# Kernel optimization log

Measured on AMD Instinct MI355X. Metric: run time of the kernel, lower is better.

## Reference

```python
import jax, jax.numpy as jnp
import numpy as np

B, D_MODEL, N, H = 2, 1024, 2048, 16
HEAD_DIM = D_MODEL // H  # 64


def _proj(x, W, b):
    # Conv1d kernel_size=1 == per-position GEMM over channels. x: [B, Cin, N]
    return jnp.einsum('oi,bin->bon', W, x) + b[:, None]


def setup_inputs() -> dict:
    key = jax.random.key(0)
    ks = jax.random.split(key, 11)
    s = 1.0 / np.sqrt(D_MODEL)
    mk = lambda k: (jax.random.uniform(k, (D_MODEL, D_MODEL), jnp.float32, -s, s))
    return {
        'query': jax.random.normal(ks[0], (B, D_MODEL, N), jnp.float32),
        'key': jax.random.normal(ks[1], (B, D_MODEL, N), jnp.float32),
        'value': jax.random.normal(ks[2], (B, D_MODEL, N), jnp.float32),
        'Wq': mk(ks[3]), 'bq': jax.random.uniform(ks[4], (D_MODEL,), jnp.float32, -s, s),
        'Wk': mk(ks[5]), 'bk': jax.random.uniform(ks[6], (D_MODEL,), jnp.float32, -s, s),
        'Wv': mk(ks[7]), 'bv': jax.random.uniform(ks[8], (D_MODEL,), jnp.float32, -s, s),
        'Wm': mk(ks[9]), 'bm': jax.random.uniform(ks[10], (D_MODEL,), jnp.float32, -s, s),
    }


def reference(query, key, value, Wq, bq, Wk, bk, Wv, bv, Wm, bm):
    b = query.shape[0]
    # project then split channels as (head_dim, heads) exactly like torch .view
    q = _proj(query, Wq, bq).reshape(b, HEAD_DIM, H, -1)  # [B, d, H, N]
    k = _proj(key, Wk, bk).reshape(b, HEAD_DIM, H, -1)
    v = _proj(value, Wv, bv).reshape(b, HEAD_DIM, H, -1)
    scores = jnp.einsum('bdhn,bdhm->bhnm', q, k) / np.sqrt(HEAD_DIM).astype(np.float32)
    prob = jax.nn.softmax(scores, axis=-1)  # [B, H, N, N]
    x = jnp.einsum('bhnm,bdhm->bdhn', prob, v)  # [B, d, H, N]
    return _proj(x.reshape(b, D_MODEL, -1), Wm, bm)  # [B, d_model, N]
```

## Files before the change

kernel.cpp:

```cpp
#include <hip/hip_runtime.h>
#include <hip/hip_bf16.h>
#include <stdint.h>

#define DM 1024
#define NS 2048
#define NH 16
#define HD 64

typedef unsigned short u16;
typedef __attribute__((ext_vector_type(8))) short short8;
typedef __attribute__((ext_vector_type(4))) short s16x4;
typedef __attribute__((ext_vector_type(8))) unsigned short u16x8;
typedef __attribute__((ext_vector_type(4))) float f32x4;
typedef __attribute__((ext_vector_type(4))) unsigned short u16x4;

#define MFMA_PV(a, b, c) __builtin_amdgcn_mfma_f32_16x16x16bf16_1k(a, b, c, 0, 0, 0)

static __device__ __forceinline__ u16 f2bf(float f) {
  union { float f; uint32_t i; } x; x.f = f;
  return (u16)((x.i + 0x7fffu + ((x.i >> 16) & 1u)) >> 16);
}
static __device__ __forceinline__ uint32_t pkbf(float a, float b) {
  union { __hip_bfloat162 h; uint32_t u; } cv;
  cv.h = __float22bfloat162_rn(float2{a, b});
  return cv.u;
}
static __device__ __forceinline__ u16x4 pkbf4(float a, float b, float c, float d) {
  union { uint32_t u[2]; u16x4 v; } cv;
  cv.u[0] = pkbf(a, b); cv.u[1] = pkbf(c, d);
  return cv.v;
}
static __device__ __forceinline__ s16x4 pkbf4s(float a, float b, float c, float d) {
  union { uint32_t u[2]; s16x4 v; } cv;
  cv.u[0] = pkbf(a, b); cv.u[1] = pkbf(c, d);
  return cv.v;
}
static __device__ __forceinline__ void gload16(u16* lds, const u16* g) {
  auto l = (__attribute__((address_space(3))) uint32_t*)(uint32_t)(uintptr_t)lds;
  auto gp = (const __attribute__((address_space(1))) uint32_t*)(uintptr_t)g;
  __builtin_amdgcn_global_load_lds(gp, l, 16, 0, 0);
}

__global__ __launch_bounds__(256) void cvt4_k(const float* __restrict__ a,
                                              const float* __restrict__ b,
                                              const float* __restrict__ c,
                                              const float* __restrict__ d,
                                              u16* __restrict__ oa, u16* __restrict__ ob,
                                              u16* __restrict__ oc, u16* __restrict__ od) {
  const int y = blockIdx.y;
  const float* in = y == 0 ? a : y == 1 ? b : y == 2 ? c : d;
  u16* out = y == 0 ? oa : y == 1 ? ob : y == 2 ? oc : od;
  int i = (blockIdx.x * 256 + threadIdx.x) * 4;
  f32x4 v = *(const f32x4*)(in + i);
  *(u16x4*)(out + i) = pkbf4(v.x, v.y, v.z, v.w);
}

__global__ __launch_bounds__(256) void trf3_k(const float* __restrict__ q,
                                              const float* __restrict__ k,
                                              const float* __restrict__ v,
                                              u16* __restrict__ oq, u16* __restrict__ ok,
                                              u16* __restrict__ ov) {
  __shared__ __attribute__((aligned(16))) u16 t[64][65];
  const int z = blockIdx.z, b = z & 1, which = z >> 1;
  const float* in = which == 0 ? q : which == 1 ? k : v;
  u16* out = which == 0 ? oq : which == 1 ? ok : ov;
  const float* ip = in + (size_t)b * DM * NS;
  u16* op = out + (size_t)b * DM * NS;
  const int r0 = blockIdx.y * 64, c0 = blockIdx.x * 64;
  const int tx = threadIdx.x, ty = threadIdx.y;
#pragma unroll
  for (int j = 0; j < 4; ++j) {
    int row = ty + j * 16;
    f32x4 vv = *(const f32x4*)(ip + (size_t)(r0 + row) * NS + c0 + tx * 4);
    u16x4 bb = pkbf4(vv.x, vv.y, vv.z, vv.w);
    t[row][tx * 4 + 0] = bb.x; t[row][tx * 4 + 1] = bb.y;
    t[row][tx * 4 + 2] = bb.z; t[row][tx * 4 + 3] = bb.w;
  }
  __syncthreads();
#pragma unroll
  for (int j = 0; j < 4; ++j) {
    int crow = ty + j * 16;
    u16x4 vv;
    vv.x = t[tx * 4 + 0][crow]; vv.y = t[tx * 4 + 1][crow];
    vv.z = t[tx * 4 + 2][crow]; vv.w = t[tx * 4 + 3][crow];
    *(u16x4*)(op + (size_t)(c0 + crow) * DM + r0 + tx * 4) = vv;
  }
}

__global__ __launch_bounds__(256) void tr_k(const u16* __restrict__ in,
                                            u16* __restrict__ out) {
  __shared__ __attribute__((aligned(16))) u16 t[64][65];
  const int b = blockIdx.z;
  const u16* ip = in + (size_t)b * DM * NS;
  u16* op = out + (size_t)b * DM * NS;
  const int r0 = blockIdx.y * 64, c0 = blockIdx.x * 64;
  const int tx = threadIdx.x, ty = threadIdx.y;
#pragma unroll
  for (int j = 0; j < 4; ++j) {
    int row = ty + j * 16;
    u16x4 v = *(const u16x4*)(ip + (size_t)(r0 + row) * NS + c0 + tx * 4);
    t[row][tx * 4 + 0] = v.x; t[row][tx * 4 + 1] = v.y;
    t[row][tx * 4 + 2] = v.z; t[row][tx * 4 + 3] = v.w;
  }
  __syncthreads();
#pragma unroll
  for (int j = 0; j < 4; ++j) {
    int crow = ty + j * 16;
    u16x4 v;
    v.x = t[tx * 4 + 0][crow]; v.y = t[tx * 4 + 1][crow];
    v.z = t[tx * 4 + 2][crow]; v.w = t[tx * 4 + 3][crow];
    *(u16x4*)(op + (size_t)(c0 + crow) * DM + r0 + tx * 4) = v;
  }
}

__global__ __launch_bounds__(256) void qkv_k(
    const u16* __restrict__ Xq, const u16* __restrict__ Xk, const u16* __restrict__ Xv,
    const u16* __restrict__ Wq, const u16* __restrict__ Wk, const u16* __restrict__ Wv,
    const float* __restrict__ bq, const float* __restrict__ bk, const float* __restrict__ bv,
    u16* __restrict__ QH, u16* __restrict__ KH, u16* __restrict__ VH) {
  __shared__ __attribute__((aligned(16))) u16 As[128 * 32];
  __shared__ __attribute__((aligned(16))) u16 Bs[128 * 32];
  const int z = blockIdx.z, b = z & 1, which = z >> 1;
  const u16* X = which == 0 ? Xq : which == 1 ? Xk : Xv;
  const u16* W = which == 0 ? Wq : which == 1 ? Wk : Wv;
  const float* bias = which == 0 ? bq : which == 1 ? bk : bv;
  u16* out = which == 0 ? QH : which == 1 ? KH : VH;
  const float sc = which == 0 ? 0.18033688011112042f : 1.0f;
  const int m0 = blockIdx.x * 128;
  const int c0 = blockIdx.y * 128;
  const u16* Xb = X + (size_t)b * NS * DM;
  const int tid = threadIdx.x;
  const int lane = tid & 63, w = tid >> 6;
  const int wm = w >> 1, wc = w & 1;
  const int qd = lane >> 4, ml = lane & 15;
  const int sml = (ml >> 1) & 3;

  f32x4 acc[4][4];
#pragma unroll
  for (int i = 0; i < 4; ++i)
#pragma unroll
    for (int j = 0; j < 4; ++j) acc[i][j] = (f32x4){0.f, 0.f, 0.f, 0.f};

  for (int k0 = 0; k0 < DM; k0 += 32) {
    __syncthreads();
#pragma unroll
    for (int it = 0; it < 2; ++it) {
      int ci = it * 256 + tid;
      int row = ci >> 2;
      int jg = (ci & 3) ^ ((ci >> 3) & 3);
      gload16(&As[ci * 8], Xb + (size_t)(m0 + row) * DM + k0 + jg * 8);
      gload16(&Bs[ci * 8], W + (size_t)(c0 + row) * DM + k0 + jg * 8);
    }
    __syncthreads();
    short8 af[4], bf[4];
#pragma unroll
    for (int i = 0; i < 4; ++i) {
      af[i] = *(const short8*)&As[(wm * 64 + i * 16 + ml) * 32 + ((qd ^ sml) * 8)];
      bf[i] = *(const short8*)&Bs[(wc * 64 + i * 16 + ml) * 32 + ((qd ^ sml) * 8)];
    }
#pragma unroll
    for (int mi = 0; mi < 4; ++mi)
#pragma unroll
      for (int ci2 = 0; ci2 < 4; ++ci2)
        acc[mi][ci2] = __builtin_amdgcn_mfma_f32_16x16x32_bf16(af[mi], bf[ci2],
                                                               acc[mi][ci2], 0, 0, 0);
  }

  const int cw = c0 + wc * 64;
  const int mw = m0 + wm * 64;
  float bv4[4];
#pragma unroll
  for (int ci2 = 0; ci2 < 4; ++ci2) bv4[ci2] = bias[cw + ci2 * 16 + ml];

  if (which < 2) {
    const int h = ml, d0 = cw >> 4;
    u16* ob = out + ((size_t)(b * NH + h) * NS) * HD;
#pragma unroll
    for (int mi = 0; mi < 4; ++mi) {
#pragma unroll
      for (int r = 0; r < 4; ++r) {
        int n = mw + mi * 16 + qd * 4 + r;
        *(u16x4*)(ob + (size_t)n * HD + d0) =
            pkbf4((acc[mi][0][r] + bv4[0]) * sc, (acc[mi][1][r] + bv4[1]) * sc,
                  (acc[mi][2][r] + bv4[2]) * sc, (acc[mi][3][r] + bv4[3]) * sc);
      }
    }
  } else {
#pragma unroll
    for (int ci2 = 0; ci2 < 4; ++ci2) {
      int c = cw + ci2 * 16 + ml;
      int h = c & 15, d = c >> 4;
#pragma unroll
      for (int mi = 0; mi < 4; ++mi) {
        int nb = mw + mi * 16 + qd * 4;
        *(u16x4*)(out + ((size_t)(b * NH + h) * HD + d) * NS + nb) =
            pkbf4(acc[mi][ci2][0] + bv4[ci2], acc[mi][ci2][1] + bv4[ci2],
                  acc[mi][ci2][2] + bv4[ci2], acc[mi][ci2][3] + bv4[ci2]);
      }
    }
  }
}

__global__ __launch_bounds__(256) void proj_o(const u16* __restrict__ X,
                                              const u16* __restrict__ W,
                                              const float* __restrict__ bias,
                                              float* __restrict__ out) {
  __shared__ __attribute__((aligned(16))) u16 As[64 * 32];
  __shared__ __attribute__((aligned(16))) u16 Bs[128 * 32];
  const int b = blockIdx.z;
  const int m0 = blockIdx.x * 64;
  const int c0 = blockIdx.y * 128;
  const u16* Xb = X + (size_t)b * NS * DM;
  const int tid = threadIdx.x;
  const int lane = tid & 63, w = tid >> 6;
  const int wm = w >> 1, wc = w & 1;
  const int qd = lane >> 4, ml = lane & 15;
  const int sml = (ml >> 1) & 3;

  f32x4 acc[2][4];
#pragma unroll
  for (int i = 0; i < 2; ++i)
#pragma unroll
    for (int j = 0; j < 4; ++j) acc[i][j] = (f32x4){0.f, 0.f, 0.f, 0.f};

  for (int k0 = 0; k0 < DM; k0 += 32) {
    __syncthreads();
    {
      int jg = (tid & 3) ^ ((tid >> 3) & 3);
      int row = tid >> 2;
      gload16(&As[tid * 8], Xb + (size_t)(m0 + row) * DM + k0 + jg * 8);
    }
#pragma unroll
    for (int it = 0; it < 2; ++it) {
      int ci = it * 256 + tid;
      int row = ci >> 2;
      int jg = (ci & 3) ^ ((ci >> 3) & 3);
      gload16(&Bs[ci * 8], W + (size_t)(c0 + row) * DM + k0 + jg * 8);
    }
    __syncthreads();
    short8 af[2], bf[4];
#pragma unroll
    for (int i = 0; i < 2; ++i)
      af[i] = *(const short8*)&As[(wm * 32 + i * 16 + ml) * 32 + ((qd ^ sml) * 8)];
#pragma unroll
    for (int i = 0; i < 4; ++i)
      bf[i] = *(const short8*)&Bs[(wc * 64 + i * 16 + ml) * 32 + ((qd ^ sml) * 8)];
#pragma unroll
    for (int mi = 0; mi < 2; ++mi)
#pragma unroll
      for (int ci2 = 0; ci2 < 4; ++ci2)
        acc[mi][ci2] = __builtin_amdgcn_mfma_f32_16x16x32_bf16(af[mi], bf[ci2],
                                                               acc[mi][ci2], 0, 0, 0);
  }

  const int cw = c0 + wc * 64;
  const int mw = m0 + wm * 32;
#pragma unroll
  for (int ci2 = 0; ci2 < 4; ++ci2) {
    int c = cw + ci2 * 16 + ml;
    float bv = bias[c];
#pragma unroll
    for (int mi = 0; mi < 2; ++mi) {
      int nb = mw + mi * 16 + qd * 4;
      f32x4 v;
      v.x = acc[mi][ci2][0] + bv; v.y = acc[mi][ci2][1] + bv;
      v.z = acc[mi][ci2][2] + bv; v.w = acc[mi][ci2][3] + bv;
      *(f32x4*)(out + ((size_t)b * DM + c) * NS + nb) = v;
    }
  }
}

__global__ __launch_bounds__(256) void attn_k(const u16* __restrict__ Q,
                                              const u16* __restrict__ K,
                                              const u16* __restrict__ V,
                                              u16* __restrict__ XO) {
  __shared__ __attribute__((aligned(16))) u16 Ks[2 * 2 * 2048];
  __shared__ __attribute__((aligned(16))) u16 Vs[2 * 2 * 2048];
  const int bh = blockIdx.y, b = bh >> 4, h = bh & 15;
  const int n0 = blockIdx.x * 64;
  const u16* Qb = Q + (size_t)bh * NS * HD;
  const u16* Kb = K + (size_t)bh * NS * HD;
  const u16* Vb = V + (size_t)bh * HD * NS;
  const int tid = threadIdx.x, lane = tid & 63, w = tid >> 6;
  const int qd = lane >> 4, ml = lane & 15;
  const int sml = (ml >> 1) & 3;

  short8 aq[2];
  {
    const u16* qr = Qb + (size_t)(n0 + w * 16 + ml) * HD + qd * 8;
    aq[0] = *(const short8*)qr;
    aq[1] = *(const short8*)(qr + 32);
  }

  const int srow = tid >> 2;
  const int jg = (tid & 3) ^ ((tid >> 3) & 3);

#pragma unroll
  for (int s = 0; s < 2; ++s) {
    gload16(&Ks[s * 2048 + tid * 8], Kb + (size_t)srow * HD + s * 32 + jg * 8);
    gload16(&Vs[s * 2048 + tid * 8], Vb + (size_t)srow * NS + s * 32 + jg * 8);
  }
  __syncthreads();

  f32x4 O[4];
#pragma unroll
  for (int i = 0; i < 4; ++i) O[i] = (f32x4){0.f, 0.f, 0.f, 0.f};
  f32x4 lsum4 = (f32x4){0.f, 0.f, 0.f, 0.f};

  for (int kb = 0; kb < NS / 64; ++kb) {
    const int cur = kb & 1, nxt = cur ^ 1;
    if (kb < NS / 64 - 1) {
#pragma unroll
      for (int s = 0; s < 2; ++s) {
        gload16(&Ks[(nxt * 2 + s) * 2048 + tid * 8],
                Kb + (size_t)((kb + 1) * 64 + srow) * HD + s * 32 + jg * 8);
        gload16(&Vs[(nxt * 2 + s) * 2048 + tid * 8],
                Vb + (size_t)srow * NS + (kb + 1) * 64 + s * 32 + jg * 8);
      }
    }

    const u16* kbase = &Ks[cur * 2 * 2048];
    f32x4 S[4];
#pragma unroll
    for (int f = 0; f < 4; ++f) S[f] = (f32x4){0.f, 0.f, 0.f, 0.f};
#pragma unroll
    for (int f = 0; f < 4; ++f)
#pragma unroll
      for (int ks = 0; ks < 2; ++ks) {
        short8 bk = *(const short8*)&kbase[ks * 2048 + (f * 16 + ml) * 32 +
                                           ((qd ^ sml) * 8)];
        S[f] = __builtin_amdgcn_mfma_f32_16x16x32_bf16(bk, aq[ks], S[f], 0, 0, 0);
      }

    s16x4 pf[4];
#pragma unroll
    for (int f = 0; f < 4; ++f) {
      f32x4 p;
      p.x = __builtin_amdgcn_exp2f(S[f][0]);
      p.y = __builtin_amdgcn_exp2f(S[f][1]);
      p.z = __builtin_amdgcn_exp2f(S[f][2]);
      p.w = __builtin_amdgcn_exp2f(S[f][3]);
      lsum4 += p;
      pf[f] = pkbf4s(p.x, p.y, p.z, p.w);
    }

    const u16* vbase = &Vs[cur * 2 * 2048];
#pragma unroll
    for (int t = 0; t < 4; ++t) {
      const int vs = t >> 1;
      const int voff = ((((t & 1) * 2 + (qd >> 1)) ^ sml) * 8) + (qd & 1) * 4;
#pragma unroll
      for (int df = 0; df < 4; ++df) {
        s16x4 vb = *(const s16x4*)&vbase[vs * 2048 + (df * 16 + ml) * 32 + voff];
        O[df] = MFMA_PV(pf[t], vb, O[df]);
      }
    }
    __syncthreads();
  }

  float lsum = (lsum4.x + lsum4.y) + (lsum4.z + lsum4.w);
  lsum += __shfl_xor(lsum, 16);
  lsum += __shfl_xor(lsum, 32);
  float linv[4];
#pragma unroll
  for (int r = 0; r < 4; ++r) linv[r] = 1.f / __shfl(lsum, qd * 4 + r);

  const int nb = n0 + w * 16 + qd * 4;
#pragma unroll
  for (int df = 0; df < 4; ++df) {
    int d = df * 16 + ml;
    int c = d * NH + h;
    *(u16x4*)(XO + ((size_t)b * DM + c) * NS + nb) =
        pkbf4(O[df][0] * linv[0], O[df][1] * linv[1],
              O[df][2] * linv[2], O[df][3] * linv[3]);
  }
}

extern "C" void kernel_launch(void* const* d_in, const int* in_sizes, int n_in,
                              void* d_out, int out_size, void* d_ws, size_t ws_size,
                              hipStream_t stream) {
  const float* query = (const float*)d_in[0];
  const float* key = (const float*)d_in[1];
  const float* value = (const float*)d_in[2];
  const float* Wq = (const float*)d_in[3]; const float* bq = (const float*)d_in[4];
  const float* Wk = (const float*)d_in[5]; const float* bk = (const float*)d_in[6];
  const float* Wv = (const float*)d_in[7]; const float* bv = (const float*)d_in[8];
  const float* Wm = (const float*)d_in[9]; const float* bm = (const float*)d_in[10];

  u16* ws = (u16*)d_ws;
  const size_t TS = (size_t)2 * NS * DM;
  const size_t WSZ = (size_t)DM * DM;
  u16* XTq = ws;
  u16* XTk = ws + TS;
  u16* XTv = ws + 2 * TS;
  u16* QH = ws + 3 * TS;
  u16* KH = ws + 4 * TS;
  u16* VH = ws + 5 * TS;
  u16* Wqb = ws + 6 * TS;
  u16* Wkb = Wqb + WSZ;
  u16* Wvb = Wkb + WSZ;
  u16* Wmb = Wvb + WSZ;
  u16* XO = XTq;
  u16* XOT = XTk;

  cvt4_k<<<dim3(WSZ / 1024, 4), 256, 0, stream>>>(Wq, Wk, Wv, Wm, Wqb, Wkb, Wvb, Wmb);

  dim3 tb(16, 16);
  trf3_k<<<dim3(NS / 64, DM / 64, 6), tb, 0, stream>>>(query, key, value, XTq, XTk, XTv);

  qkv_k<<<dim3(NS / 128, DM / 128, 6), 256, 0, stream>>>(
      XTq, XTk, XTv, Wqb, Wkb, Wvb, bq, bk, bv, QH, KH, VH);

  attn_k<<<dim3(NS / 64, 32), 256, 0, stream>>>(QH, KH, VH, XO);

  tr_k<<<dim3(NS / 64, DM / 64, 2), tb, 0, stream>>>(XO, XOT);
  proj_o<<<dim3(NS / 64, DM / 128, 2), 256, 0, stream>>>(XOT, Wmb, bm, (float*)d_out);
}
```

Before: 244.0 us.

## Write attention output token-major and permute Wm columns to drop transpose kernel

```diff
diff --git a/kernel.cpp b/kernel.cpp
--- a/kernel.cpp
+++ b/kernel.cpp
@@ -16,10 +16,6 @@
 
 #define MFMA_PV(a, b, c) __builtin_amdgcn_mfma_f32_16x16x16bf16_1k(a, b, c, 0, 0, 0)
 
-static __device__ __forceinline__ u16 f2bf(float f) {
-  union { float f; uint32_t i; } x; x.f = f;
-  return (u16)((x.i + 0x7fffu + ((x.i >> 16) & 1u)) >> 16);
-}
 static __device__ __forceinline__ uint32_t pkbf(float a, float b) {
   union { __hip_bfloat162 h; uint32_t u; } cv;
   cv.h = __float22bfloat162_rn(float2{a, b});
@@ -41,18 +37,46 @@
   __builtin_amdgcn_global_load_lds(gp, l, 16, 0, 0);
 }
 
-__global__ __launch_bounds__(256) void cvt4_k(const float* __restrict__ a,
+__global__ __launch_bounds__(256) void cvt3_k(const float* __restrict__ a,
                                               const float* __restrict__ b,
                                               const float* __restrict__ c,
-                                              const float* __restrict__ d,
                                               u16* __restrict__ oa, u16* __restrict__ ob,
-                                              u16* __restrict__ oc, u16* __restrict__ od) {
+                                              u16* __restrict__ oc) {
   const int y = blockIdx.y;
-  const float* in = y == 0 ? a : y == 1 ? b : y == 2 ? c : d;
-  u16* out = y == 0 ? oa : y == 1 ? ob : y == 2 ? oc : od;
+  const float* in = y == 0 ? a : y == 1 ? b : c;
+  u16* out = y == 0 ? oa : y == 1 ? ob : oc;
   int i = (blockIdx.x * 256 + threadIdx.x) * 4;
   f32x4 v = *(const f32x4*)(in + i);
   *(u16x4*)(out + i) = pkbf4(v.x, v.y, v.z, v.w);
+}
+
+__global__ __launch_bounds__(256) void cvtp_k(const float* __restrict__ in,
+                                              u16* __restrict__ out) {
+  __shared__ __attribute__((aligned(16))) u16 t[4][16][68];
+  const int tid = threadIdx.x;
+  const int rr = tid >> 6, tl = tid & 63;
+  const int row = blockIdx.x * 4 + rr;
+  const float* ip = in + (size_t)row * DM;
+  u16* op = out + (size_t)row * DM;
+#pragma unroll
+  for (int e = 0; e < 4; ++e) {
+    int i = e * 256 + tl * 4;
+    f32x4 v = *(const f32x4*)(ip + i);
+    u16x4 bb = pkbf4(v.x, v.y, v.z, v.w);
+    int d = i >> 4, h0 = i & 15;
+    t[rr][h0 + 0][d] = bb.x; t[rr][h0 + 1][d] = bb.y;
+    t[rr][h0 + 2][d] = bb.z; t[rr][h0 + 3][d] = bb.w;
+  }
+  __syncthreads();
+#pragma unroll
+  for (int e = 0; e < 4; ++e) {
+    int j = e * 256 + tl * 4;
+    int h = j >> 6, d = j & 63;
+    u16x4 v;
+    v.x = t[rr][h][d + 0]; v.y = t[rr][h][d + 1];
+    v.z = t[rr][h][d + 2]; v.w = t[rr][h][d + 3];
+    *(u16x4*)(op + j) = v;
+  }
 }
 
 __global__ __launch_bounds__(256) void trf3_k(const float* __restrict__ q,
@@ -84,32 +108,6 @@
     vv.x = t[tx * 4 + 0][crow]; vv.y = t[tx * 4 + 1][crow];
     vv.z = t[tx * 4 + 2][crow]; vv.w = t[tx * 4 + 3][crow];
     *(u16x4*)(op + (size_t)(c0 + crow) * DM + r0 + tx * 4) = vv;
-  }
-}
-
-__global__ __launch_bounds__(256) void tr_k(const u16* __restrict__ in,
-                                            u16* __restrict__ out) {
-  __shared__ __attribute__((aligned(16))) u16 t[64][65];
-  const int b = blockIdx.z;
-  const u16* ip = in + (size_t)b * DM * NS;
-  u16* op = out + (size_t)b * DM * NS;
-  const int r0 = blockIdx.y * 64, c0 = blockIdx.x * 64;
-  const int tx = threadIdx.x, ty = threadIdx.y;
-#pragma unroll
-  for (int j = 0; j < 4; ++j) {
-    int row = ty + j * 16;
-    u16x4 v = *(const u16x4*)(ip + (size_t)(r0 + row) * NS + c0 + tx * 4);
-    t[row][tx * 4 + 0] = v.x; t[row][tx * 4 + 1] = v.y;
-    t[row][tx * 4 + 2] = v.z; t[row][tx * 4 + 3] = v.w;
-  }
-  __syncthreads();
-#pragma unroll
-  for (int j = 0; j < 4; ++j) {
-    int crow = ty + j * 16;
-    u16x4 v;
-    v.x = t[tx * 4 + 0][crow]; v.y = t[tx * 4 + 1][crow];
-    v.z = t[tx * 4 + 2][crow]; v.w = t[tx * 4 + 3][crow];
-    *(u16x4*)(op + (size_t)(c0 + crow) * DM + r0 + tx * 4) = v;
   }
 }
 
@@ -352,7 +350,7 @@
 #pragma unroll
       for (int df = 0; df < 4; ++df) {
         s16x4 vb = *(const s16x4*)&vbase[vs * 2048 + (df * 16 + ml) * 32 + voff];
-        O[df] = MFMA_PV(pf[t], vb, O[df]);
+        O[df] = MFMA_PV(vb, pf[t], O[df]);
       }
     }
     __syncthreads();
@@ -361,18 +359,13 @@
   float lsum = (lsum4.x + lsum4.y) + (lsum4.z + lsum4.w);
   lsum += __shfl_xor(lsum, 16);
   lsum += __shfl_xor(lsum, 32);
-  float linv[4];
-#pragma unroll
-  for (int r = 0; r < 4; ++r) linv[r] = 1.f / __shfl(lsum, qd * 4 + r);
-
-  const int nb = n0 + w * 16 + qd * 4;
+  const float linv = 1.f / lsum;
+
+  u16* xb = XO + ((size_t)(b * NS) + n0 + w * 16 + ml) * DM + h * 64;
 #pragma unroll
   for (int df = 0; df < 4; ++df) {
-    int d = df * 16 + ml;
-    int c = d * NH + h;
-    *(u16x4*)(XO + ((size_t)b * DM + c) * NS + nb) =
-        pkbf4(O[df][0] * linv[0], O[df][1] * linv[1],
-              O[df][2] * linv[2], O[df][3] * linv[3]);
+    *(u16x4*)(xb + df * 16 + qd * 4) =
+        pkbf4(O[df][0] * linv, O[df][1] * linv, O[df][2] * linv, O[df][3] * linv);
   }
 }
 
@@ -401,9 +394,9 @@
   u16* Wvb = Wkb + WSZ;
   u16* Wmb = Wvb + WSZ;
   u16* XO = XTq;
-  u16* XOT = XTk;
-
-  cvt4_k<<<dim3(WSZ / 1024, 4), 256, 0, stream>>>(Wq, Wk, Wv, Wm, Wqb, Wkb, Wvb, Wmb);
+
+  cvt3_k<<<dim3(WSZ / 1024, 3), 256, 0, stream>>>(Wq, Wk, Wv, Wqb, Wkb, Wvb);
+  cvtp_k<<<DM / 4, 256, 0, stream>>>(Wm, Wmb);
 
   dim3 tb(16, 16);
   trf3_k<<<dim3(NS / 64, DM / 64, 6), tb, 0, stream>>>(query, key, value, XTq, XTk, XTv);
@@ -413,6 +406,5 @@
 
   attn_k<<<dim3(NS / 64, 32), 256, 0, stream>>>(QH, KH, VH, XO);
 
-  tr_k<<<dim3(NS / 64, DM / 64, 2), tb, 0, stream>>>(XO, XOT);
-  proj_o<<<dim3(NS / 64, DM / 128, 2), 256, 0, stream>>>(XOT, Wmb, bm, (float*)d_out);
-}
+  proj_o<<<dim3(NS / 64, DM / 128, 2), 256, 0, stream>>>(XO, Wmb, bm, (float*)d_out);
+}
```

Measured after the change: 237.3 us. 1.03x faster.
